# Kernel tuning notes

Measured on AMD Instinct MI355X. Metric: run time of the kernel, lower is better.

## Reference

```python
import jax, jax.numpy as jnp
import numpy as np

SIGMA = 0.5   # pairwise density bandwidth (density_std)
EPS = 1e-8
B, N, K, P, D, F, H = 8, 20, 2, 320, 3, 64, 64


def setup_inputs() -> dict:
    key = jax.random.key(0)
    ks = jax.random.split(key, 8)
    # ring graph: neighbor node index for each of the K=2 incident slots
    nbr = np.stack([(np.arange(N) - 1) % N, (np.arange(N) + 1) % N], axis=1).astype(np.int32)
    return {
        "X": jax.random.uniform(ks[0], (B, N, K, P, D), minval=-1.0, maxval=1.0),
        "W": jax.random.uniform(ks[1], (B, N, K, P), minval=0.1, maxval=1.0),
        "feats": jax.random.normal(ks[2], (B, N, F)),
        "mu": 0.1 * jax.random.normal(ks[3], (N, K, D)),
        "W1": jax.random.normal(ks[4], (N, F, H)) / np.sqrt(F),
        "Wx": jax.random.normal(ks[5], (N, D, H)) / np.sqrt(D),
        "b1": jnp.zeros((N, H), jnp.float32),
        "W2": jax.random.normal(ks[6], (N, H)) / np.sqrt(H),
        "bias2": jnp.zeros((N,), jnp.float32),
        "nbr_idx": jnp.asarray(nbr),
    }


def reference(X, W, feats, mu, W1, Wx, b1, W2, bias2, nbr_idx):
    # X: [B,N,K,P,D] belief/message particles, W: [B,N,K,P] particle weights
    Bs, Ns, Ks, Ps, Ds = X.shape
    KP = Ks * Ps
    # normalize incoming message weights per node (as in uniform_init: sum over K*P == 1)
    Wn = W / (W.sum(axis=(2, 3), keepdims=True) + EPS)
    Xf = X.reshape(Bs, Ns, KP, Ds)
    Wf = Wn.reshape(Bs, Ns, KP)
    # irregular gather of each node's neighbors' particles/weights
    Xn = Xf[:, nbr_idx]   # [B,N,K,KP,D]
    Wnb = Wf[:, nbr_idx]  # [B,N,K,KP]
    # pairwise edge density: Gaussian on (x_dst - mu_e) vs x_src, via ||a||^2+||b||^2-2ab
    a = X - mu[None, :, :, None, :]                      # [B,N,K,P,D]
    cross = jnp.einsum('bnkpd,bnkqd->bnkpq', a, Xn)      # [B,N,K,P,KP]
    d2 = (a * a).sum(-1)[..., None] + (Xn * Xn).sum(-1)[..., None, :] - 2.0 * cross
    kern = jnp.exp(-d2 / (2.0 * SIGMA * SIGMA))
    # neighbor message: weighted density sum over neighbor particles
    msg = jnp.einsum('bnkpq,bnkq->bnkp', kern, Wnb)      # [B,N,K,P]
    # per-node unary likelihood MLP on (image features, particle state)
    hf = jnp.einsum('bnf,nfh->bnh', feats, W1)           # [B,N,H]
    hx = jnp.einsum('bnkpd,ndh->bnkph', X, Wx)           # [B,N,K,P,H]
    h = jax.nn.relu(hf[:, :, None, None, :] + hx + b1[None, :, None, None, :])
    u = jax.nn.sigmoid(jnp.einsum('bnkph,nh->bnkp', h, W2) + bias2[None, :, None, None])
    # belief weight update: unary * neighbor message, renormalized per node
    w = u * msg
    return w / (w.sum(axis=(2, 3), keepdims=True) + EPS)
```

## Files before the change

### kernel.cpp

```cpp
#include <hip/hip_runtime.h>
#include <hip/hip_bf16.h>

constexpr int B_ = 8, N_ = 20, K_ = 2, P_ = 320, D_ = 3, F_ = 64, H_ = 64;
constexpr int Q_ = K_ * P_;
constexpr float EPS_ = 1e-8f;
constexpr float LOG2E_ = 1.4426950408889634f;

__global__ __launch_bounds__(Q_) void dnbp_kernel(
    const float* __restrict__ X,
    const float* __restrict__ W,
    const float* __restrict__ feats,
    const float* __restrict__ mu,
    const float* __restrict__ W1,
    const float* __restrict__ Wx,
    const float* __restrict__ b1,
    const float* __restrict__ W2,
    const float* __restrict__ bias2,
    const int* __restrict__ nbr,
    float* __restrict__ out)
{
    __shared__ float4 xn4[K_][Q_];
    __shared__ float4 wx4[H_];
    __shared__ float  hb[H_];
    __shared__ float  red[2 * 10];
    __shared__ float  sumW[2];
    __shared__ float  totalS;

    const int bn  = blockIdx.x;
    const int b   = bn / N_;
    const int n   = bn - b * N_;
    const int tid = threadIdx.x;
    const int wave = tid >> 6;
    const int lane = tid & 63;

    const int j0 = nbr[n * 2 + 0];
    const int j1 = nbr[n * 2 + 1];

    if (tid < H_) {
        const int h = tid;
        const float* fp  = feats + ((size_t)b * N_ + n) * F_;
        const float* w1p = W1 + (size_t)n * F_ * H_ + h;
        float acc = 0.f;
        #pragma unroll 8
        for (int f = 0; f < F_; ++f)
            acc = fmaf(fp[f], w1p[(size_t)f * H_], acc);
        hb[h] = acc + b1[n * H_ + h];
        const float* wxp = Wx + (size_t)n * D_ * H_ + h;
        wx4[h] = make_float4(wxp[0], wxp[H_], wxp[2 * H_], W2[n * H_ + h]);
    }

    const int q = tid;
    float w0, w1;
    {
        const size_t base0 = ((size_t)b * N_ + j0) * Q_ + q;
        const float* xp = X + base0 * D_;
        const float x0 = xp[0], x1 = xp[1], x2 = xp[2];
        const float sq = x0 * x0 + x1 * x1 + x2 * x2;
        w0 = W[base0];
        xn4[0][q] = make_float4(x0, x1, x2,
                                w0 * __builtin_amdgcn_exp2f(-2.f * LOG2E_ * sq));
    }
    {
        const size_t base1 = ((size_t)b * N_ + j1) * Q_ + q;
        const float* xp = X + base1 * D_;
        const float x0 = xp[0], x1 = xp[1], x2 = xp[2];
        const float sq = x0 * x0 + x1 * x1 + x2 * x2;
        w1 = W[base1];
        xn4[1][q] = make_float4(x0, x1, x2,
                                w1 * __builtin_amdgcn_exp2f(-2.f * LOG2E_ * sq));
    }

    {
        float v0 = w0, v1 = w1;
        #pragma unroll
        for (int off = 32; off > 0; off >>= 1) {
            v0 += __shfl_down(v0, off, 64);
            v1 += __shfl_down(v1, off, 64);
        }
        if (lane == 0) { red[wave * 2] = v0; red[wave * 2 + 1] = v1; }
        __syncthreads();
        if (tid == 0) {
            float s0 = 0.f, s1 = 0.f;
            #pragma unroll
            for (int wv = 0; wv < 10; ++wv) { s0 += red[wv * 2]; s1 += red[wv * 2 + 1]; }
            sumW[0] = 1.f / (s0 + EPS_);
            sumW[1] = 1.f / (s1 + EPS_);
        }
        __syncthreads();
    }

    xn4[0][q].w *= sumW[0];
    xn4[1][q].w *= sumW[1];
    __syncthreads();

    const int k = (tid >= P_) ? 1 : 0;
    const int p = tid - k * P_;
    const size_t rowbase = (((size_t)b * N_ + n) * K_ + k) * P_ + p;
    const float* xp = X + rowbase * D_;
    const float x0 = xp[0], x1 = xp[1], x2 = xp[2];
    const float* mup = mu + (n * K_ + k) * D_;
    const float a0 = x0 - mup[0];
    const float a1 = x1 - mup[1];
    const float a2 = x2 - mup[2];
    const float ra2 = a0 * a0 + a1 * a1 + a2 * a2;
    const float s0 = a0 * (4.f * LOG2E_);
    const float s1 = a1 * (4.f * LOG2E_);
    const float s2 = a2 * (4.f * LOG2E_);

    float acc = bias2[n];
    #pragma unroll 8
    for (int h = 0; h < H_; ++h) {
        const float4 wv = wx4[h];
        float t = fmaf(x0, wv.x, fmaf(x1, wv.y, fmaf(x2, wv.z, hb[h])));
        t = fmaxf(t, 0.f);
        acc = fmaf(t, wv.w, acc);
    }
    const float u = 1.f / (1.f + __expf(-acc));

    const float4* __restrict__ xk = xn4[k];
    float m0 = 0.f, m1 = 0.f, m2 = 0.f, m3 = 0.f;
    #pragma unroll 2
    for (int qq = 0; qq < Q_; qq += 4) {
        const float4 f0 = xk[qq];
        const float4 f1 = xk[qq + 1];
        const float4 f2 = xk[qq + 2];
        const float4 f3 = xk[qq + 3];
        const float d0 = fmaf(s0, f0.x, fmaf(s1, f0.y, s2 * f0.z));
        const float d1 = fmaf(s0, f1.x, fmaf(s1, f1.y, s2 * f1.z));
        const float d2 = fmaf(s0, f2.x, fmaf(s1, f2.y, s2 * f2.z));
        const float d3 = fmaf(s0, f3.x, fmaf(s1, f3.y, s2 * f3.z));
        m0 = fmaf(f0.w, __builtin_amdgcn_exp2f(d0), m0);
        m1 = fmaf(f1.w, __builtin_amdgcn_exp2f(d1), m1);
        m2 = fmaf(f2.w, __builtin_amdgcn_exp2f(d2), m2);
        m3 = fmaf(f3.w, __builtin_amdgcn_exp2f(d3), m3);
    }
    const float msg = ((m0 + m1) + (m2 + m3)) *
                      __builtin_amdgcn_exp2f(-2.f * LOG2E_ * ra2);
    const float wval = u * msg;

    {
        float v = wval;
        #pragma unroll
        for (int off = 32; off > 0; off >>= 1) v += __shfl_down(v, off, 64);
        if (lane == 0) red[wave] = v;
        __syncthreads();
        if (tid == 0) {
            float s = 0.f;
            #pragma unroll
            for (int wv = 0; wv < 10; ++wv) s += red[wv];
            totalS = 1.f / (s + EPS_);
        }
        __syncthreads();
    }

    out[((size_t)b * N_ + n) * Q_ + tid] = wval * totalS;
}

extern "C" void kernel_launch(void* const* d_in, const int* in_sizes, int n_in,
                              void* d_out, int out_size, void* d_ws, size_t ws_size,
                              hipStream_t stream) {
    const float* X     = (const float*)d_in[0];
    const float* W     = (const float*)d_in[1];
    const float* feats = (const float*)d_in[2];
    const float* mu    = (const float*)d_in[3];
    const float* W1    = (const float*)d_in[4];
    const float* Wx    = (const float*)d_in[5];
    const float* b1    = (const float*)d_in[6];
    const float* W2    = (const float*)d_in[7];
    const float* bias2 = (const float*)d_in[8];
    const int*   nbr   = (const int*)d_in[9];
    float*       out   = (float*)d_out;

    dnbp_kernel<<<B_ * N_, Q_, 0, stream>>>(X, W, feats, mu, W1, Wx, b1, W2,
                                            bias2, nbr, out);
}
```

Measured before the change: 96.88 us.

## Repack shared particle data for packed FP32 FMA in message and MLP loops

Reorganizes the neighbor-particle and MLP weight tables in shared memory into pair-interleaved float4 arrays so that two particles (or two hidden units) can be processed per v_pk_fma_f32 via inline asm. The per-row ra2 term is folded into the exponent argument instead of being applied as a final multiply. The aim is to halve the VALU FMA instruction count in the exp-bound inner loops. The exp2 calls stay scalar, the fmax is done per lane, and the inline asm may limit compiler scheduling.

```diff
diff --git a/kernel.cpp b/kernel.cpp
--- a/kernel.cpp
+++ b/kernel.cpp
@@ -5,6 +5,16 @@
 constexpr int Q_ = K_ * P_;
 constexpr float EPS_ = 1e-8f;
 constexpr float LOG2E_ = 1.4426950408889634f;
+
+typedef float v2f __attribute__((ext_vector_type(2)));
+
+__device__ __forceinline__ v2f mk2(float a, float b) { v2f r; r.x = a; r.y = b; return r; }
+
+__device__ __forceinline__ v2f pk_fma(v2f a, v2f b, v2f c) {
+    v2f d;
+    asm("v_pk_fma_f32 %0, %1, %2, %3" : "=v"(d) : "v"(a), "v"(b), "v"(c));
+    return d;
+}
 
 __global__ __launch_bounds__(Q_) void dnbp_kernel(
     const float* __restrict__ X,
@@ -19,9 +29,11 @@
     const int* __restrict__ nbr,
     float* __restrict__ out)
 {
-    __shared__ float4 xn4[K_][Q_];
-    __shared__ float4 wx4[H_];
-    __shared__ float  hb[H_];
+    __shared__ float4 xnA[K_][Q_ / 2];
+    __shared__ float4 xnB[K_][Q_ / 2];
+    __shared__ float4 gA[H_ / 2];
+    __shared__ float4 gB[H_ / 2];
+    __shared__ v2f    hb2[H_ / 2];
     __shared__ float  red[2 * 10];
     __shared__ float  sumW[2];
     __shared__ float  totalS;
@@ -44,30 +56,41 @@
         #pragma unroll 8
         for (int f = 0; f < F_; ++f)
             acc = fmaf(fp[f], w1p[(size_t)f * H_], acc);
-        hb[h] = acc + b1[n * H_ + h];
+        const int hi = h >> 1, ho = h & 1;
+        ((float*)&hb2[hi])[ho] = acc + b1[n * H_ + h];
         const float* wxp = Wx + (size_t)n * D_ * H_ + h;
-        wx4[h] = make_float4(wxp[0], wxp[H_], wxp[2 * H_], W2[n * H_ + h]);
-    }
-
-    const int q = tid;
-    float w0, w1;
+        float* ga = (float*)&gA[hi];
+        float* gb = (float*)&gB[hi];
+        ga[ho]     = wxp[0];
+        ga[2 + ho] = wxp[H_];
+        gb[ho]     = wxp[2 * H_];
+        gb[2 + ho] = W2[n * H_ + h];
+    }
+
+    const int q  = tid;
+    const int qi = q >> 1, qo = q & 1;
+    float w0, w1, ew0, ew1;
     {
         const size_t base0 = ((size_t)b * N_ + j0) * Q_ + q;
         const float* xp = X + base0 * D_;
         const float x0 = xp[0], x1 = xp[1], x2 = xp[2];
         const float sq = x0 * x0 + x1 * x1 + x2 * x2;
-        w0 = W[base0];
-        xn4[0][q] = make_float4(x0, x1, x2,
-                                w0 * __builtin_amdgcn_exp2f(-2.f * LOG2E_ * sq));
+        w0  = W[base0];
+        ew0 = __builtin_amdgcn_exp2f(-2.f * LOG2E_ * sq);
+        float* a  = (float*)&xnA[0][qi];
+        float* bq = (float*)&xnB[0][qi];
+        a[qo] = x0; a[2 + qo] = x1; bq[qo] = x2;
     }
     {
         const size_t base1 = ((size_t)b * N_ + j1) * Q_ + q;
         const float* xp = X + base1 * D_;
         const float x0 = xp[0], x1 = xp[1], x2 = xp[2];
         const float sq = x0 * x0 + x1 * x1 + x2 * x2;
-        w1 = W[base1];
-        xn4[1][q] = make_float4(x0, x1, x2,
-                                w1 * __builtin_amdgcn_exp2f(-2.f * LOG2E_ * sq));
+        w1  = W[base1];
+        ew1 = __builtin_amdgcn_exp2f(-2.f * LOG2E_ * sq);
+        float* a  = (float*)&xnA[1][qi];
+        float* bq = (float*)&xnB[1][qi];
+        a[qo] = x0; a[2 + qo] = x1; bq[qo] = x2;
     }
 
     {
@@ -89,8 +112,8 @@
         __syncthreads();
     }
 
-    xn4[0][q].w *= sumW[0];
-    xn4[1][q].w *= sumW[1];
+    ((float*)&xnB[0][qi])[2 + qo] = w0 * ew0 * sumW[0];
+    ((float*)&xnB[1][qi])[2 + qo] = w1 * ew1 * sumW[1];
     __syncthreads();
 
     const int k = (tid >= P_) ? 1 : 0;
@@ -103,39 +126,47 @@
     const float a1 = x1 - mup[1];
     const float a2 = x2 - mup[2];
     const float ra2 = a0 * a0 + a1 * a1 + a2 * a2;
-    const float s0 = a0 * (4.f * LOG2E_);
-    const float s1 = a1 * (4.f * LOG2E_);
-    const float s2 = a2 * (4.f * LOG2E_);
-
-    float acc = bias2[n];
-    #pragma unroll 8
-    for (int h = 0; h < H_; ++h) {
-        const float4 wv = wx4[h];
-        float t = fmaf(x0, wv.x, fmaf(x1, wv.y, fmaf(x2, wv.z, hb[h])));
-        t = fmaxf(t, 0.f);
-        acc = fmaf(t, wv.w, acc);
-    }
-    const float u = 1.f / (1.f + __expf(-acc));
-
-    const float4* __restrict__ xk = xn4[k];
-    float m0 = 0.f, m1 = 0.f, m2 = 0.f, m3 = 0.f;
+    const v2f S0 = mk2(a0 * (4.f * LOG2E_), a0 * (4.f * LOG2E_));
+    const v2f S1 = mk2(a1 * (4.f * LOG2E_), a1 * (4.f * LOG2E_));
+    const v2f S2 = mk2(a2 * (4.f * LOG2E_), a2 * (4.f * LOG2E_));
+    const v2f RA = mk2(-2.f * LOG2E_ * ra2, -2.f * LOG2E_ * ra2);
+
+    const v2f X0v = mk2(x0, x0), X1v = mk2(x1, x1), X2v = mk2(x2, x2);
+    v2f acc2 = mk2(0.f, 0.f);
+    #pragma unroll 4
+    for (int i = 0; i < H_ / 2; ++i) {
+        const float4 ga = gA[i];
+        const float4 gb = gB[i];
+        const v2f   hb = hb2[i];
+        v2f t = pk_fma(X0v, mk2(ga.x, ga.y),
+                pk_fma(X1v, mk2(ga.z, ga.w),
+                pk_fma(X2v, mk2(gb.x, gb.y), hb)));
+        t.x = fmaxf(t.x, 0.f);
+        t.y = fmaxf(t.y, 0.f);
+        acc2 = pk_fma(t, mk2(gb.z, gb.w), acc2);
+    }
+    const float logit = bias2[n] + acc2.x + acc2.y;
+    const float u = 1.f / (1.f + __expf(-logit));
+
+    const float4* __restrict__ pA = xnA[k];
+    const float4* __restrict__ pB = xnB[k];
+    v2f m0 = mk2(0.f, 0.f), m1 = mk2(0.f, 0.f);
     #pragma unroll 2
-    for (int qq = 0; qq < Q_; qq += 4) {
-        const float4 f0 = xk[qq];
-        const float4 f1 = xk[qq + 1];
-        const float4 f2 = xk[qq + 2];
-        const float4 f3 = xk[qq + 3];
-        const float d0 = fmaf(s0, f0.x, fmaf(s1, f0.y, s2 * f0.z));
-        const float d1 = fmaf(s0, f1.x, fmaf(s1, f1.y, s2 * f1.z));
-        const float d2 = fmaf(s0, f2.x, fmaf(s1, f2.y, s2 * f2.z));
-        const float d3 = fmaf(s0, f3.x, fmaf(s1, f3.y, s2 * f3.z));
-        m0 = fmaf(f0.w, __builtin_amdgcn_exp2f(d0), m0);
-        m1 = fmaf(f1.w, __builtin_amdgcn_exp2f(d1), m1);
-        m2 = fmaf(f2.w, __builtin_amdgcn_exp2f(d2), m2);
-        m3 = fmaf(f3.w, __builtin_amdgcn_exp2f(d3), m3);
-    }
-    const float msg = ((m0 + m1) + (m2 + m3)) *
-                      __builtin_amdgcn_exp2f(-2.f * LOG2E_ * ra2);
+    for (int t2 = 0; t2 < Q_ / 2; t2 += 2) {
+        const float4 A0 = pA[t2], A1 = pA[t2 + 1];
+        const float4 B0 = pB[t2], B1 = pB[t2 + 1];
+        v2f d0 = pk_fma(mk2(A0.x, A0.y), S0,
+                 pk_fma(mk2(A0.z, A0.w), S1,
+                 pk_fma(mk2(B0.x, B0.y), S2, RA)));
+        v2f d1 = pk_fma(mk2(A1.x, A1.y), S0,
+                 pk_fma(mk2(A1.z, A1.w), S1,
+                 pk_fma(mk2(B1.x, B1.y), S2, RA)));
+        v2f e0 = mk2(__builtin_amdgcn_exp2f(d0.x), __builtin_amdgcn_exp2f(d0.y));
+        v2f e1 = mk2(__builtin_amdgcn_exp2f(d1.x), __builtin_amdgcn_exp2f(d1.y));
+        m0 = pk_fma(mk2(B0.z, B0.w), e0, m0);
+        m1 = pk_fma(mk2(B1.z, B1.w), e1, m1);
+    }
+    const float msg = (m0.x + m0.y) + (m1.x + m1.y);
     const float wval = u * msg;
 
     {
```

Result: no change. 96.50 us (-0.4%).

## Split each node into row tiles across blocks with a separate normalization kernel

Applied to the files above, without the earlier changes.

The grid grows from 160 to 1600 blocks by giving each block 64 rows of one node/slot. Within a block, 16 threads cooperate on each group of 4 rows over the 640 neighbor particles, and their partial sums are reduced through shared memory. The final per-node renormalization moves to a second small kernel that reads per-tile partial sums from the workspace. This aims to fill the GPU's many CUs and raise per-thread ILP, at the cost of redundantly recomputing the neighbor staging and the hf projection in every tile, plus an extra launch and global round trip.

```diff
diff --git a/kernel.cpp b/kernel.cpp
--- a/kernel.cpp
+++ b/kernel.cpp
@@ -1,12 +1,13 @@
 #include <hip/hip_runtime.h>
-#include <hip/hip_bf16.h>
 
 constexpr int B_ = 8, N_ = 20, K_ = 2, P_ = 320, D_ = 3, F_ = 64, H_ = 64;
 constexpr int Q_ = K_ * P_;
 constexpr float EPS_ = 1e-8f;
 constexpr float LOG2E_ = 1.4426950408889634f;
+constexpr int TILES_ = 10;
+constexpr int ROWS_  = 64;
 
-__global__ __launch_bounds__(Q_) void dnbp_kernel(
+__global__ __launch_bounds__(256) void main_kernel(
     const float* __restrict__ X,
     const float* __restrict__ W,
     const float* __restrict__ feats,
@@ -17,143 +18,141 @@
     const float* __restrict__ W2,
     const float* __restrict__ bias2,
     const int* __restrict__ nbr,
+    float* __restrict__ wsPart,
     float* __restrict__ out)
 {
-    __shared__ float4 xn4[K_][Q_];
-    __shared__ float4 wx4[H_];
-    __shared__ float  hb[H_];
-    __shared__ float  red[2 * 10];
-    __shared__ float  sumW[2];
-    __shared__ float  totalS;
+    __shared__ float4 sQ[Q_];
+    __shared__ float4 aT[ROWS_];
+    __shared__ float4 xT[ROWS_];
+    __shared__ float4 gT[H_];
+    __shared__ float  hbT[H_];
+    __shared__ float  part[ROWS_][17];
+    __shared__ float  red[4];
+    __shared__ float  invW;
 
-    const int bn  = blockIdx.x;
-    const int b   = bn / N_;
-    const int n   = bn - b * N_;
-    const int tid = threadIdx.x;
+    const int blk  = blockIdx.x;
+    const int bn   = blk / TILES_;
+    const int tile = blk - bn * TILES_;
+    const int b    = bn / N_;
+    const int n    = bn - b * N_;
+    const int tid  = threadIdx.x;
     const int wave = tid >> 6;
     const int lane = tid & 63;
+    const int k    = (tile >= 5) ? 1 : 0;
+    const int r0   = tile * ROWS_;
+    const int j    = nbr[n * 2 + k];
 
-    const int j0 = nbr[n * 2 + 0];
-    const int j1 = nbr[n * 2 + 1];
+    const size_t nbase = ((size_t)b * N_ + j) * Q_;
+    float wsum = 0.f;
+    for (int i = tid; i < Q_; i += 256) {
+        const float* xp = X + (nbase + i) * D_;
+        const float x0 = xp[0], x1 = xp[1], x2 = xp[2];
+        const float sq = x0 * x0 + x1 * x1 + x2 * x2;
+        const float w  = W[nbase + i];
+        const float c  = w * __builtin_amdgcn_exp2f(-2.f * LOG2E_ * sq);
+        sQ[i] = make_float4(x0, x1, x2, c);
+        wsum += w;
+    }
+    {
+        float v = wsum;
+        #pragma unroll
+        for (int off = 32; off > 0; off >>= 1) v += __shfl_down(v, off, 64);
+        if (lane == 0) red[wave] = v;
+    }
 
-    if (tid < H_) {
+    if (tid < ROWS_) {
+        const int gr = r0 + tid;
+        const float* xp = X + ((size_t)bn * Q_ + gr) * D_;
+        const float x0 = xp[0], x1 = xp[1], x2 = xp[2];
+        const float* mup = mu + (n * K_ + k) * D_;
+        const float a0 = x0 - mup[0];
+        const float a1 = x1 - mup[1];
+        const float a2 = x2 - mup[2];
+        const float ra2 = a0 * a0 + a1 * a1 + a2 * a2;
+        aT[tid] = make_float4(a0 * (4.f * LOG2E_), a1 * (4.f * LOG2E_),
+                              a2 * (4.f * LOG2E_), -2.f * LOG2E_ * ra2);
+        xT[tid] = make_float4(x0, x1, x2, 0.f);
+
         const int h = tid;
-        const float* fp  = feats + ((size_t)b * N_ + n) * F_;
+        const float* fp  = feats + (size_t)bn * F_;
         const float* w1p = W1 + (size_t)n * F_ * H_ + h;
         float acc = 0.f;
         #pragma unroll 8
         for (int f = 0; f < F_; ++f)
             acc = fmaf(fp[f], w1p[(size_t)f * H_], acc);
-        hb[h] = acc + b1[n * H_ + h];
+        hbT[h] = acc + b1[n * H_ + h];
         const float* wxp = Wx + (size_t)n * D_ * H_ + h;
-        wx4[h] = make_float4(wxp[0], wxp[H_], wxp[2 * H_], W2[n * H_ + h]);
+        gT[h] = make_float4(wxp[0], wxp[H_], wxp[2 * H_], W2[n * H_ + h]);
     }
-
-    const int q = tid;
-    float w0, w1;
-    {
-        const size_t base0 = ((size_t)b * N_ + j0) * Q_ + q;
-        const float* xp = X + base0 * D_;
-        const float x0 = xp[0], x1 = xp[1], x2 = xp[2];
-        const float sq = x0 * x0 + x1 * x1 + x2 * x2;
-        w0 = W[base0];
-        xn4[0][q] = make_float4(x0, x1, x2,
-                                w0 * __builtin_amdgcn_exp2f(-2.f * LOG2E_ * sq));
-    }
-    {
-        const size_t base1 = ((size_t)b * N_ + j1) * Q_ + q;
-        const float* xp = X + base1 * D_;
-        const float x0 = xp[0], x1 = xp[1], x2 = xp[2];
-        const float sq = x0 * x0 + x1 * x1 + x2 * x2;
-        w1 = W[base1];
-        xn4[1][q] = make_float4(x0, x1, x2,
-                                w1 * __builtin_amdgcn_exp2f(-2.f * LOG2E_ * sq));
-    }
-
-    {
-        float v0 = w0, v1 = w1;
-        #pragma unroll
-        for (int off = 32; off > 0; off >>= 1) {
-            v0 += __shfl_down(v0, off, 64);
-            v1 += __shfl_down(v1, off, 64);
-        }
-        if (lane == 0) { red[wave * 2] = v0; red[wave * 2 + 1] = v1; }
-        __syncthreads();
-        if (tid == 0) {
-            float s0 = 0.f, s1 = 0.f;
-            #pragma unroll
-            for (int wv = 0; wv < 10; ++wv) { s0 += red[wv * 2]; s1 += red[wv * 2 + 1]; }
-            sumW[0] = 1.f / (s0 + EPS_);
-            sumW[1] = 1.f / (s1 + EPS_);
-        }
-        __syncthreads();
-    }
-
-    xn4[0][q].w *= sumW[0];
-    xn4[1][q].w *= sumW[1];
     __syncthreads();
 
-    const int k = (tid >= P_) ? 1 : 0;
-    const int p = tid - k * P_;
-    const size_t rowbase = (((size_t)b * N_ + n) * K_ + k) * P_ + p;
-    const float* xp = X + rowbase * D_;
-    const float x0 = xp[0], x1 = xp[1], x2 = xp[2];
-    const float* mup = mu + (n * K_ + k) * D_;
-    const float a0 = x0 - mup[0];
-    const float a1 = x1 - mup[1];
-    const float a2 = x2 - mup[2];
-    const float ra2 = a0 * a0 + a1 * a1 + a2 * a2;
-    const float s0 = a0 * (4.f * LOG2E_);
-    const float s1 = a1 * (4.f * LOG2E_);
-    const float s2 = a2 * (4.f * LOG2E_);
+    if (tid == 0)
+        invW = 1.f / (((red[0] + red[1]) + (red[2] + red[3])) + EPS_);
 
-    float acc = bias2[n];
-    #pragma unroll 8
-    for (int h = 0; h < H_; ++h) {
-        const float4 wv = wx4[h];
-        float t = fmaf(x0, wv.x, fmaf(x1, wv.y, fmaf(x2, wv.z, hb[h])));
-        t = fmaxf(t, 0.f);
-        acc = fmaf(t, wv.w, acc);
+    const int g = tid >> 4;
+    const int s = tid & 15;
+    float S0[4], S1[4], S2[4], RA[4], acc[4];
+    #pragma unroll
+    for (int jj = 0; jj < 4; ++jj) {
+        const float4 av = aT[g * 4 + jj];
+        S0[jj] = av.x; S1[jj] = av.y; S2[jj] = av.z; RA[jj] = av.w;
+        acc[jj] = 0.f;
     }
-    const float u = 1.f / (1.f + __expf(-acc));
+    #pragma unroll 4
+    for (int i = 0; i < Q_ / 16; ++i) {
+        const float4 Pq = sQ[i * 16 + s];
+        #pragma unroll
+        for (int jj = 0; jj < 4; ++jj) {
+            const float d = fmaf(Pq.x, S0[jj],
+                            fmaf(Pq.y, S1[jj],
+                            fmaf(Pq.z, S2[jj], RA[jj])));
+            acc[jj] = fmaf(Pq.w, __builtin_amdgcn_exp2f(d), acc[jj]);
+        }
+    }
+    #pragma unroll
+    for (int jj = 0; jj < 4; ++jj)
+        part[g * 4 + jj][s] = acc[jj];
 
-    const float4* __restrict__ xk = xn4[k];
-    float m0 = 0.f, m1 = 0.f, m2 = 0.f, m3 = 0.f;
-    #pragma unroll 2
-    for (int qq = 0; qq < Q_; qq += 4) {
-        const float4 f0 = xk[qq];
-        const float4 f1 = xk[qq + 1];
-        const float4 f2 = xk[qq + 2];
-        const float4 f3 = xk[qq + 3];
-        const float d0 = fmaf(s0, f0.x, fmaf(s1, f0.y, s2 * f0.z));
-        const float d1 = fmaf(s0, f1.x, fmaf(s1, f1.y, s2 * f1.z));
-        const float d2 = fmaf(s0, f2.x, fmaf(s1, f2.y, s2 * f2.z));
-        const float d3 = fmaf(s0, f3.x, fmaf(s1, f3.y, s2 * f3.z));
-        m0 = fmaf(f0.w, __builtin_amdgcn_exp2f(d0), m0);
-        m1 = fmaf(f1.w, __builtin_amdgcn_exp2f(d1), m1);
-        m2 = fmaf(f2.w, __builtin_amdgcn_exp2f(d2), m2);
-        m3 = fmaf(f3.w, __builtin_amdgcn_exp2f(d3), m3);
-    }
-    const float msg = ((m0 + m1) + (m2 + m3)) *
-                      __builtin_amdgcn_exp2f(-2.f * LOG2E_ * ra2);
-    const float wval = u * msg;
+    __syncthreads();
 
-    {
+    if (tid < ROWS_) {
+        const int row = tid;
+        const float* pr = part[row];
+        const float msg =
+            (((pr[0] + pr[1]) + (pr[2] + pr[3])) + ((pr[4] + pr[5]) + (pr[6] + pr[7]))) +
+            (((pr[8] + pr[9]) + (pr[10] + pr[11])) + ((pr[12] + pr[13]) + (pr[14] + pr[15])));
+
+        const float4 xr = xT[row];
+        float accg = bias2[n];
+        #pragma unroll 8
+        for (int h = 0; h < H_; ++h) {
+            const float4 gv = gT[h];
+            float t = fmaf(xr.x, gv.x, fmaf(xr.y, gv.y, fmaf(xr.z, gv.z, hbT[h])));
+            t = fmaxf(t, 0.f);
+            accg = fmaf(t, gv.w, accg);
+        }
+        const float u = 1.f / (1.f + __expf(-accg));
+        const float wval = u * msg * invW;
+
+        out[(size_t)bn * Q_ + r0 + row] = wval;
+
         float v = wval;
         #pragma unroll
         for (int off = 32; off > 0; off >>= 1) v += __shfl_down(v, off, 64);
-        if (lane == 0) red[wave] = v;
-        __syncthreads();
-        if (tid == 0) {
-            float s = 0.f;
-            #pragma unroll
-            for (int wv = 0; wv < 10; ++wv) s += red[wv];
-            totalS = 1.f / (s + EPS_);
-        }
-        __syncthreads();
+        if (tid == 0) wsPart[blk] = v;
     }
+}
 
-    out[((size_t)b * N_ + n) * Q_ + tid] = wval * totalS;
+__global__ __launch_bounds__(Q_) void norm_kernel(
+    const float* __restrict__ wsPart, float* __restrict__ out)
+{
+    const int bn = blockIdx.x;
+    const float* p = wsPart + bn * TILES_;
+    float s0 = 0.f, s1 = 0.f;
+    #pragma unroll
+    for (int t = 0; t < TILES_ / 2; ++t) { s0 += p[2 * t]; s1 += p[2 * t + 1]; }
+    const float inv = 1.f / ((s0 + s1) + EPS_);
+    out[(size_t)bn * Q_ + threadIdx.x] *= inv;
 }
 
 extern "C" void kernel_launch(void* const* d_in, const int* in_sizes, int n_in,
@@ -170,7 +169,9 @@
     const float* bias2 = (const float*)d_in[8];
     const int*   nbr   = (const int*)d_in[9];
     float*       out   = (float*)d_out;
+    float*       wsPart = (float*)d_ws;
 
-    dnbp_kernel<<<B_ * N_, Q_, 0, stream>>>(X, W, feats, mu, W1, Wx, b1, W2,
-                                            bias2, nbr, out);
+    main_kernel<<<B_ * N_ * TILES_, 256, 0, stream>>>(
+        X, W, feats, mu, W1, Wx, b1, W2, bias2, nbr, wsPart, out);
+    norm_kernel<<<B_ * N_, Q_, 0, stream>>>(wsPart, out);
 }
```

Measured after the change: 91.58 us. 5.5% less time.
